# Kernel tuning notes

Measured on AMD Instinct MI355X. Metric: run time of the kernel, lower is better.

## Reference

```python
import jax, jax.numpy as jnp
import numpy as np


def setup_inputs() -> dict:
    key = jax.random.key(0)
    k1, = jax.random.split(key, 1)
    x = jax.random.normal(k1, (8, 16, 512, 512), dtype=jnp.float32)
    inv_sqrt2 = 0.7071067811865476
    g0 = jnp.array([inv_sqrt2, inv_sqrt2], dtype=jnp.float32)
    g1 = jnp.array([inv_sqrt2, -inv_sqrt2], dtype=jnp.float32)
    return {"x": x, "g0": g0, "g1": g1}


def _interleave(a, b, axis):
    # stack a/b alternately along `axis`: out[..., 2i] = a[..., i], out[..., 2i+1] = b[..., i]
    s = jnp.stack([a, b], axis=axis + 1)
    shape = list(a.shape)
    shape[axis] *= 2
    return s.reshape(shape)


def reference(x, g0, g1):
    # x: [B, 16, H, W] -> subbands, each [B, 4, H, W]
    lls, hls, lhs, hhs = x[:, 0:4], x[:, 4:8], x[:, 8:12], x[:, 12:16]
    # ConvTranspose2d with (2,1) kernel, stride (2,1): out[2i]=w[0]*in[i], out[2i+1]=w[1]*in[i]
    # lo = net1(ll) + net2(hl); hi = net1(lh) + net2(hh)  (row upsampling)
    lo = _interleave(g0[0] * lls + g1[0] * hls, g0[1] * lls + g1[1] * hls, axis=2)
    hi = _interleave(g0[0] * lhs + g1[0] * hhs, g0[1] * lhs + g1[1] * hhs, axis=2)
    # column upsampling with transposed (1,2) kernels: out = l + h
    out = _interleave(g0[0] * lo + g1[0] * hi, g0[1] * lo + g1[1] * hi, axis=3)
    return out  # [B, 4, 2H, 2W]
```

## Files before the change

kernel.cpp:

```cpp
#include <hip/hip_runtime.h>


using f2 = __attribute__((ext_vector_type(2))) float;
using f4 = __attribute__((ext_vector_type(4))) float;

__global__ __launch_bounds__(256) void FreTransferInv_kernel(
    const float* __restrict__ x,
    const float* __restrict__ g0,
    const float* __restrict__ g1,
    float* __restrict__ out)
{
    const float g00 = g0[0], g01 = g0[1];
    const float g10 = g1[0], g11 = g1[1];

    const int tid = blockIdx.x * 256 + threadIdx.x;

    const int jg = tid & 255;
    const int i  = (tid >> 8) & 511;
    const int bc = tid >> 17;
    const int b  = bc >> 2;
    const int c  = bc & 3;

    const size_t plane = 512 * 512;
    const size_t in_base =
        ((size_t)(b * 16 + c) * 512 + (size_t)i) * 512 + (size_t)jg * 2;

    const f2 lls = *(const f2*)(x + in_base);
    const f2 hls = *(const f2*)(x + in_base + 4 * plane);
    const f2 lhs = *(const f2*)(x + in_base + 8 * plane);
    const f2 hhs = *(const f2*)(x + in_base + 12 * plane);

    f4 ve, vo;
#pragma unroll
    for (int k = 0; k < 2; ++k) {
        const float L  = lls[k];
        const float H  = hls[k];
        const float Lh = lhs[k];
        const float Hh = hhs[k];
        const float lo_e = g00 * L  + g10 * H;
        const float lo_o = g01 * L  + g11 * H;
        const float hi_e = g00 * Lh + g10 * Hh;
        const float hi_o = g01 * Lh + g11 * Hh;
        ve[2 * k]     = g00 * lo_e + g10 * hi_e;
        ve[2 * k + 1] = g01 * lo_e + g11 * hi_e;
        vo[2 * k]     = g00 * lo_o + g10 * hi_o;
        vo[2 * k + 1] = g01 * lo_o + g11 * hi_o;
    }

    const size_t out_e =
        ((size_t)bc * 1024 + (size_t)(2 * i)) * 1024 + (size_t)jg * 4;

    *(f4*)(out + out_e) = ve;
    *(f4*)(out + out_e + 1024) = vo;
}

extern "C" void kernel_launch(void* const* d_in, const int* in_sizes, int n_in,
                              void* d_out, int out_size, void* d_ws, size_t ws_size,
                              hipStream_t stream) {
    const float* x  = (const float*)d_in[0];
    const float* g0 = (const float*)d_in[1];
    const float* g1 = (const float*)d_in[2];
    float* out = (float*)d_out;

    const int total_threads = 8 * 4 * 512 * 256;
    const int blocks = total_threads / 256;
    FreTransferInv_kernel<<<blocks, 256, 0, stream>>>(x, g0, g1, out);
}
```

Measured before the change: 231.0 us.

## Loop over batch per thread with prefetch and nontemporal loads/stores

New measurement: 232.8 us. About the same (+0.8%).

```diff
diff --git a/kernel.cpp b/kernel.cpp
--- a/kernel.cpp
+++ b/kernel.cpp
@@ -14,44 +14,59 @@
     const float g10 = g1[0], g11 = g1[1];
 
     const int tid = blockIdx.x * 256 + threadIdx.x;
-
-    const int jg = tid & 255;
-    const int i  = (tid >> 8) & 511;
-    const int bc = tid >> 17;
-    const int b  = bc >> 2;
-    const int c  = bc & 3;
+    const int jg  = tid & 255;
+    const int i   = (tid >> 8) & 511;
+    const int bc0 = tid >> 17;
 
     const size_t plane = 512 * 512;
-    const size_t in_base =
-        ((size_t)(b * 16 + c) * 512 + (size_t)i) * 512 + (size_t)jg * 2;
+    const float* pin  = x + ((size_t)bc0 * 512 + (size_t)i) * 512 + (size_t)jg * 2;
+    float*       pout = out + ((size_t)bc0 * 1024 + (size_t)(2 * i)) * 1024
+                            + (size_t)jg * 4;
+    const size_t in_step  = (size_t)16 * plane;
+    const size_t out_step = (size_t)4 * 1024 * 1024;
 
-    const f2 lls = *(const f2*)(x + in_base);
-    const f2 hls = *(const f2*)(x + in_base + 4 * plane);
-    const f2 lhs = *(const f2*)(x + in_base + 8 * plane);
-    const f2 hhs = *(const f2*)(x + in_base + 12 * plane);
+    f2 a0 = __builtin_nontemporal_load((const f2*)(pin));
+    f2 a1 = __builtin_nontemporal_load((const f2*)(pin + 4 * plane));
+    f2 a2 = __builtin_nontemporal_load((const f2*)(pin + 8 * plane));
+    f2 a3 = __builtin_nontemporal_load((const f2*)(pin + 12 * plane));
 
-    f4 ve, vo;
 #pragma unroll
-    for (int k = 0; k < 2; ++k) {
-        const float L  = lls[k];
-        const float H  = hls[k];
-        const float Lh = lhs[k];
-        const float Hh = hhs[k];
-        const float lo_e = g00 * L  + g10 * H;
-        const float lo_o = g01 * L  + g11 * H;
-        const float hi_e = g00 * Lh + g10 * Hh;
-        const float hi_o = g01 * Lh + g11 * Hh;
-        ve[2 * k]     = g00 * lo_e + g10 * hi_e;
-        ve[2 * k + 1] = g01 * lo_e + g11 * hi_e;
-        vo[2 * k]     = g00 * lo_o + g10 * hi_o;
-        vo[2 * k + 1] = g01 * lo_o + g11 * hi_o;
+    for (int k = 0; k < 8; ++k) {
+        f2 b0, b1, b2, b3;
+        if (k < 7) {
+            const float* pn = pin + in_step;
+            b0 = __builtin_nontemporal_load((const f2*)(pn));
+            b1 = __builtin_nontemporal_load((const f2*)(pn + 4 * plane));
+            b2 = __builtin_nontemporal_load((const f2*)(pn + 8 * plane));
+            b3 = __builtin_nontemporal_load((const f2*)(pn + 12 * plane));
+        }
+
+        f4 ve, vo;
+#pragma unroll
+        for (int kk = 0; kk < 2; ++kk) {
+            const float L  = a0[kk];
+            const float H  = a1[kk];
+            const float Lh = a2[kk];
+            const float Hh = a3[kk];
+            const float lo_e = g00 * L  + g10 * H;
+            const float lo_o = g01 * L  + g11 * H;
+            const float hi_e = g00 * Lh + g10 * Hh;
+            const float hi_o = g01 * Lh + g11 * Hh;
+            ve[2 * kk]     = g00 * lo_e + g10 * hi_e;
+            ve[2 * kk + 1] = g01 * lo_e + g11 * hi_e;
+            vo[2 * kk]     = g00 * lo_o + g10 * hi_o;
+            vo[2 * kk + 1] = g01 * lo_o + g11 * hi_o;
+        }
+
+        __builtin_nontemporal_store(ve, (f4*)(pout));
+        __builtin_nontemporal_store(vo, (f4*)(pout + 1024));
+
+        if (k < 7) {
+            a0 = b0; a1 = b1; a2 = b2; a3 = b3;
+            pin  += in_step;
+            pout += out_step;
+        }
     }
-
-    const size_t out_e =
-        ((size_t)bc * 1024 + (size_t)(2 * i)) * 1024 + (size_t)jg * 4;
-
-    *(f4*)(out + out_e) = ve;
-    *(f4*)(out + out_e + 1024) = vo;
 }
 
 extern "C" void kernel_launch(void* const* d_in, const int* in_sizes, int n_in,
@@ -62,7 +77,5 @@
     const float* g1 = (const float*)d_in[2];
     float* out = (float*)d_out;
 
-    const int total_threads = 8 * 4 * 512 * 256;
-    const int blocks = total_threads / 256;
-    FreTransferInv_kernel<<<blocks, 256, 0, stream>>>(x, g0, g1, out);
+    FreTransferInv_kernel<<<2048, 256, 0, stream>>>(x, g0, g1, out);
 }
```
